# Kernel optimization log

Measured on AMD Instinct MI355X. Metric: run time of the kernel, lower is better.

Reference implementation:

```python
import jax, jax.numpy as jnp
import numpy as np


def setup_inputs() -> dict:
    key = jax.random.key(0)
    k1, k2 = jax.random.split(key)
    B, S, D = 32, 1024, 1024
    text = jax.random.normal(k1, (B, S, D), dtype=jnp.float32)
    W = jax.random.normal(k2, (D, D), dtype=jnp.float32) * (1.0 / np.sqrt(D))
    b = jnp.zeros((D,), dtype=jnp.float32)
    return {"text": text, "W": W, "b": b}


def reference(text, W, b):
    # Q = K = V = Linear(text); torch Linear is x @ W.T + b
    D = W.shape[0]
    qkv = text @ W.T + b  # [B, S, D]
    scale = jnp.asarray(1.0 / np.sqrt(D), dtype=qkv.dtype)
    scores = jnp.einsum("bqd,bkd->bqk", qkv, qkv) * scale  # [B, S, S]
    # F.softmax(H) on a 3D tensor uses torch's legacy implicit dim=0 (batch dim)
    attn = jax.nn.softmax(scores, axis=0)
    out = jnp.einsum("bqk,bkd->bqd", attn, qkv)  # [B, S, D]
    return out
```

## Files before the change

### kernel.cpp

```cpp
#include <hip/hip_runtime.h>
#include <hip/hip_bf16.h>

typedef __attribute__((ext_vector_type(4))) float f32x4;
typedef __attribute__((ext_vector_type(8))) short short8;

static constexpr int BB = 32;
static constexpr int SEQ = 1024;
static constexpr int DIM = 1024;

__device__ __forceinline__ ushort f2bf(float f) {
  union { float f; uint u; } x; x.f = f;
  uint r = x.u + 0x7fffu + ((x.u >> 16) & 1u);
  return (ushort)(r >> 16);
}
__device__ __forceinline__ float bf2f(ushort h) {
  union { uint u; float f; } x; x.u = ((uint)h) << 16; return x.f;
}

__device__ __forceinline__ void async16(const void* g, void* l) {
  __builtin_amdgcn_global_load_lds(
      (const __attribute__((address_space(1))) unsigned int*)g,
      (__attribute__((address_space(3))) unsigned int*)l, 16, 0, 0);
}

#define SCHED0 __builtin_amdgcn_sched_barrier(0)
#define BAR    __builtin_amdgcn_s_barrier()
#define VM(n)  asm volatile("s_waitcnt vmcnt(" #n ")" ::: "memory")

__global__ void cvt_kernel(const float* __restrict__ in, ushort* __restrict__ out, long n4) {
  long i = (long)blockIdx.x * blockDim.x + threadIdx.x;
  const long stride = (long)gridDim.x * blockDim.x;
  for (; i < n4; i += stride) {
    float4 v = reinterpret_cast<const float4*>(in)[i];
    ushort4 o = make_ushort4(f2bf(v.x), f2bf(v.y), f2bf(v.z), f2bf(v.w));
    reinterpret_cast<ushort4*>(out)[i] = o;
  }
}

template<int OUT_BF16, int HAS_BIAS, int TMODE>
__global__ __launch_bounds__(512, 2)
void gemm256(const ushort* __restrict__ A, const ushort* __restrict__ Bt,
             void* __restrict__ Cv, const float* __restrict__ bias,
             ushort* __restrict__ Tout,
             int M, int N, int K, float scale,
             long sA, long sB, long sC)
{
  __shared__ __align__(16) ushort As[2][16384];
  __shared__ __align__(16) ushort Bs[2][16384];

  const int t = threadIdx.x;
  const int z = blockIdx.z;
  const ushort* Ab = A + (long)z * sA;
  const ushort* Bb = Bt + (long)z * sB;
  const int tm = blockIdx.y * 256;
  const int tn = blockIdx.x * 256;

  const int l    = t & 63;
  const int w    = t >> 6;
  const int wrow = w >> 2;
  const int wcol = w & 3;
  const int fr   = l & 15;
  const int g    = l >> 4;
  const int aflip = (fr & 7) << 4;

  const int q0 = (g << 4) ^ aflip;
  const int q1 = (64 + (g << 4)) ^ aflip;
  const char* pA0 = (const char*)As + (wrow << 13) + (fr << 7) + q0;
  const char* pA1 = (const char*)As + (wrow << 13) + (fr << 7) + q1;
  const char* pB0 = (const char*)Bs + (wcol << 12) + (fr << 7) + q0;
  const char* pB1 = (const char*)Bs + (wcol << 12) + (fr << 7) + q1;

  auto ldA = [&](int buf, int mi, int ks) -> short8 {
    const int off = (buf << 15) + ((mi >> 1 & 1) << 14) + ((mi >> 2) << 12) + ((mi & 1) << 11);
    return *(const short8*)((ks ? pA1 : pA0) + off);
  };
  auto ldB = [&](int buf, int ni, int ks) -> short8 {
    const int off = (buf << 15) + ((ni >> 1 & 1) << 14) + ((ni & 1) << 11);
    return *(const short8*)((ks ? pB1 : pB0) + off);
  };

  const long tmK = (long)tm * K;
  const long tnK = (long)tn * K;
  auto soff = [&](int j) {
    const int P  = (j << 13) + (t << 4);
    const int L  = P ^ (((P >> 7) & 7) << 4);
    const int lr = L >> 7;
    const int kb = (L & 127) >> 1;
    return (((lr >> 5) & 3) * 64 + ((lr >> 7) << 5) + (lr & 31)) * K + kb;
  };
  const long ao0 = tmK + soff(0), ao1 = tmK + soff(1), ao2 = tmK + soff(2), ao3 = tmK + soff(3);
  const long bo0 = tnK + soff(0), bo1 = tnK + soff(1), bo2 = tnK + soff(2), bo3 = tnK + soff(3);
  const int t16 = t << 4;
  auto stgA = [&](int buf, int j, long go, int koff) {
    async16(Ab + go + koff, (char*)As + (buf << 15) + (j << 13) + t16);
  };
  auto stgB = [&](int buf, int j, long go, int koff) {
    async16(Bb + go + koff, (char*)Bs + (buf << 15) + (j << 13) + t16);
  };

  f32x4 acc[8][4];
#pragma unroll
  for (int i = 0; i < 8; ++i)
#pragma unroll
    for (int j = 0; j < 4; ++j) acc[i][j] = {0.f, 0.f, 0.f, 0.f};

  short8 a0[4][2], a1[4][2], b0[2][2], b1[2][2];
  constexpr int MI0[4] = {0, 1, 4, 5};
  constexpr int MI1[4] = {2, 3, 6, 7};

#define MFMA_Q(ASET, MIARR, BSET, NIOFF)                                        \
  __builtin_amdgcn_s_setprio(1);                                                \
  _Pragma("unroll") for (int ks = 0; ks < 2; ++ks)                              \
  _Pragma("unroll") for (int s = 0; s < 4; ++s)                                 \
  _Pragma("unroll") for (int ni = 0; ni < 2; ++ni)                              \
    acc[MIARR[s]][ni + NIOFF] = __builtin_amdgcn_mfma_f32_16x16x32_bf16(        \
        ASET[s][ks], BSET[ni][ks], acc[MIARR[s]][ni + NIOFF], 0, 0, 0);         \
  __builtin_amdgcn_s_setprio(0);

  const int NKT = K >> 6;

  stgA(0, 0, ao0, 0);  stgA(0, 1, ao1, 0);
  stgB(0, 0, bo0, 0);  stgB(0, 1, bo1, 0);
  stgB(0, 2, bo2, 0);  stgB(0, 3, bo3, 0);
  stgA(0, 2, ao2, 0);  stgA(0, 3, ao3, 0);
  stgA(1, 0, ao0, 64); stgA(1, 1, ao1, 64);
  stgB(1, 0, bo0, 64); stgB(1, 1, bo1, 64);
  stgB(1, 2, bo2, 64); stgB(1, 3, bo3, 64);
  VM(8);
  BAR;

#pragma unroll
  for (int s = 0; s < 4; ++s) { a0[s][0] = ldA(0, MI0[s], 0); a0[s][1] = ldA(0, MI0[s], 1); }
#pragma unroll
  for (int ni = 0; ni < 2; ++ni) { b0[ni][0] = ldB(0, ni, 0); b0[ni][1] = ldB(0, ni, 1); }

#pragma unroll 2
  for (int kt = 0; kt < NKT; ++kt) {
    const int buf = kt & 1;
    const bool h1 = (kt + 1) < NKT;
    const bool h2 = (kt + 2) < NKT;
    const int k1 = (kt + 1) << 6;
    const int k2 = (kt + 2) << 6;

#pragma unroll
    for (int ni = 0; ni < 2; ++ni) { b1[ni][0] = ldB(buf, ni + 2, 0); b1[ni][1] = ldB(buf, ni + 2, 1); }
    if (h1) { stgA(buf ^ 1, 2, ao2, k1); stgA(buf ^ 1, 3, ao3, k1); }
    SCHED0;
    MFMA_Q(a0, MI0, b0, 0);
    if (kt < NKT - 1) { VM(8); } else { VM(0); }
    BAR;

#pragma unroll
    for (int s = 0; s < 4; ++s) { a1[s][0] = ldA(buf, MI1[s], 0); a1[s][1] = ldA(buf, MI1[s], 1); }
    if (h2) { stgA(buf, 0, ao0, k2); stgA(buf, 1, ao1, k2); }
    SCHED0;
    MFMA_Q(a0, MI0, b1, 2);
    if (kt < NKT - 2) { VM(8); } else if (kt == NKT - 2) { VM(6); }
    BAR;

    if (h1) {
#pragma unroll
      for (int s = 0; s < 4; ++s) { a0[s][0] = ldA(buf ^ 1, MI0[s], 0); a0[s][1] = ldA(buf ^ 1, MI0[s], 1); }
    }
    if (h2) { stgB(buf, 0, bo0, k2); stgB(buf, 1, bo1, k2); }
    SCHED0;
    MFMA_Q(a1, MI1, b0, 0);
    if (kt < NKT - 2) { VM(8); } else if (kt == NKT - 2) { VM(4); }
    BAR;

    if (h1) {
#pragma unroll
      for (int ni = 0; ni < 2; ++ni) { b0[ni][0] = ldB(buf ^ 1, ni, 0); b0[ni][1] = ldB(buf ^ 1, ni, 1); }
    }
    if (h2) { stgB(buf, 2, bo2, k2); stgB(buf, 3, bo3, k2); }
    SCHED0;
    MFMA_Q(a1, MI1, b1, 2);
    if (kt < NKT - 2) { VM(8); } else if (kt == NKT - 2) { VM(2); }
    BAR;
  }
#undef MFMA_Q

  const int cr = g * 4;
#pragma unroll
  for (int mi = 0; mi < 8; ++mi) {
#pragma unroll
    for (int ni = 0; ni < 4; ++ni) {
      const int row = tm + wrow * 128 + mi * 16 + cr;
      const int col = tn + wcol * 64 + ni * 16 + fr;
      const float bv = HAS_BIAS ? bias[col] : 0.0f;
      float v[4];
#pragma unroll
      for (int r = 0; r < 4; ++r) v[r] = acc[mi][ni][r] * scale + bv;
#pragma unroll
      for (int r = 0; r < 4; ++r) {
        const long off = (long)z * sC + (long)(row + r) * N + col;
        if (OUT_BF16) ((ushort*)Cv)[off] = f2bf(v[r]);
        else          ((float*)Cv)[off]  = v[r];
      }
      if (TMODE) {
        ushort4 o = make_ushort4(f2bf(v[0]), f2bf(v[1]), f2bf(v[2]), f2bf(v[3]));
        const long ti = ((long)(row >> 10) << 20) + ((long)col << 10) + (row & 1023);
        *(ushort4*)&Tout[ti] = o;
      }
    }
  }
}

__global__ void softmax_b(ushort* __restrict__ sc) {
  const long SSl = (long)SEQ * SEQ;
  const long e = ((long)blockIdx.x * blockDim.x + threadIdx.x) * 4;
  if (e >= SSl) return;
  uint2 raw[BB];
#pragma unroll
  for (int b = 0; b < BB; ++b) raw[b] = *(const uint2*)&sc[b * SSl + e];
  float mx[4] = {-3.0e38f, -3.0e38f, -3.0e38f, -3.0e38f};
#pragma unroll
  for (int b = 0; b < BB; ++b) {
    const uint lo = raw[b].x, hi = raw[b].y;
    mx[0] = fmaxf(mx[0], bf2f((ushort)(lo & 0xffffu)));
    mx[1] = fmaxf(mx[1], bf2f((ushort)(lo >> 16)));
    mx[2] = fmaxf(mx[2], bf2f((ushort)(hi & 0xffffu)));
    mx[3] = fmaxf(mx[3], bf2f((ushort)(hi >> 16)));
  }
  float sum[4] = {0.f, 0.f, 0.f, 0.f};
#pragma unroll
  for (int b = 0; b < BB; ++b) {
    const uint lo = raw[b].x, hi = raw[b].y;
    const float x0 = __expf(bf2f((ushort)(lo & 0xffffu)) - mx[0]);
    const float x1 = __expf(bf2f((ushort)(lo >> 16))     - mx[1]);
    const float x2 = __expf(bf2f((ushort)(hi & 0xffffu)) - mx[2]);
    const float x3 = __expf(bf2f((ushort)(hi >> 16))     - mx[3]);
    sum[0] += x0; sum[1] += x1; sum[2] += x2; sum[3] += x3;
    raw[b].x = (uint)f2bf(x0) | ((uint)f2bf(x1) << 16);
    raw[b].y = (uint)f2bf(x2) | ((uint)f2bf(x3) << 16);
  }
  const float r0 = 1.0f / sum[0], r1 = 1.0f / sum[1];
  const float r2 = 1.0f / sum[2], r3 = 1.0f / sum[3];
#pragma unroll
  for (int b = 0; b < BB; ++b) {
    const uint lo = raw[b].x, hi = raw[b].y;
    const uint o0 = f2bf(bf2f((ushort)(lo & 0xffffu)) * r0);
    const uint o1 = f2bf(bf2f((ushort)(lo >> 16))     * r1);
    const uint o2 = f2bf(bf2f((ushort)(hi & 0xffffu)) * r2);
    const uint o3 = f2bf(bf2f((ushort)(hi >> 16))     * r3);
    uint2 o; o.x = o0 | (o1 << 16); o.y = o2 | (o3 << 16);
    *(uint2*)&sc[b * SSl + e] = o;
  }
}

extern "C" void kernel_launch(void* const* d_in, const int* in_sizes, int n_in,
                              void* d_out, int out_size, void* d_ws, size_t ws_size,
                              hipStream_t stream) {
  const float* text = (const float*)d_in[0];
  const float* W    = (const float*)d_in[1];
  const float* bias = (const float*)d_in[2];
  float* out = (float*)d_out;

  const long nTxt = (long)BB * SEQ * DIM;
  const long nW   = (long)DIM * DIM;
  const long SSl  = (long)SEQ * SEQ;

  char* ws = (char*)d_ws;
  ushort* qkv   = (ushort*)ws;
  ushort* qkvT  = (ushort*)(ws + nTxt * 2);
  ushort* sc    = (ushort*)(ws + nTxt * 4);
  ushort* textb = sc;
  ushort* Wb    = (ushort*)(ws + nTxt * 6);
  if (ws_size < (size_t)(nTxt * 6 + nW * 2)) return;

  cvt_kernel<<<2048, 256, 0, stream>>>(text, textb, nTxt / 4);
  cvt_kernel<<<256, 256, 0, stream>>>(W, Wb, nW / 4);
  gemm256<1, 1, 1><<<dim3(4, 128, 1), 512, 0, stream>>>(
      textb, Wb, qkv, bias, qkvT, BB * SEQ, DIM, DIM, 1.0f, 0, 0, 0);
  gemm256<1, 0, 0><<<dim3(4, 4, BB), 512, 0, stream>>>(
      qkv, qkv, sc, nullptr, nullptr, SEQ, SEQ, DIM, 0.03125f, SSl, SSl, SSl);
  softmax_b<<<1024, 256, 0, stream>>>(sc);
  gemm256<0, 0, 0><<<dim3(4, 4, BB), 512, 0, stream>>>(
      sc, qkvT, out, nullptr, nullptr, SEQ, DIM, SEQ, 1.0f, SSl, SSl, SSl);
}
```

Before: 376.3 us.

## Exploit score symmetry with triangular-tile GEMM and XCD-aware block remapping

Adds a 128x128-tile GEMM that computes only the lower-triangular tiles of the symmetric Q·Q^T score matrix and mirrors each off-diagonal tile via transposed bf16 stores, roughly halving the score GEMM's MFMA work. All GEMMs now use a 1D grid with a block-index swizzle that spreads consecutive logical tiles across the 8 XCDs for better L2 locality. The transposed mirror writes are strided and uncoalesced, and the triangular index decode uses a per-block loop.

```diff
diff --git a/kernel.cpp b/kernel.cpp
--- a/kernel.cpp
+++ b/kernel.cpp
@@ -42,19 +42,25 @@
 void gemm256(const ushort* __restrict__ A, const ushort* __restrict__ Bt,
              void* __restrict__ Cv, const float* __restrict__ bias,
              ushort* __restrict__ Tout,
-             int M, int N, int K, float scale,
+             int nx, int ny, int K, float scale,
              long sA, long sB, long sC)
 {
   __shared__ __align__(16) ushort As[2][16384];
   __shared__ __align__(16) ushort Bs[2][16384];
 
-  const int t = threadIdx.x;
-  const int z = blockIdx.z;
+  const int lg = (blockIdx.x & 7) * (gridDim.x >> 3) + (blockIdx.x >> 3);
+  const int tx = lg % nx;
+  const int rr = lg / nx;
+  const int ty = rr % ny;
+  const int z  = rr / ny;
+  const int N  = nx * 256;
+  const int tm = ty * 256;
+  const int tn = tx * 256;
+
   const ushort* Ab = A + (long)z * sA;
   const ushort* Bb = Bt + (long)z * sB;
-  const int tm = blockIdx.y * 256;
-  const int tn = blockIdx.x * 256;
-
+
+  const int t = threadIdx.x;
   const int l    = t & 63;
   const int w    = t >> 6;
   const int wrow = w >> 2;
@@ -206,6 +212,109 @@
   }
 }
 
+template<int OUT_BF16, int HAS_BIAS, int SYM>
+__global__ void gemm_bt(const ushort* __restrict__ A, const ushort* __restrict__ Bt,
+                        void* __restrict__ Cv, const float* __restrict__ bias,
+                        int nx, int ny, int K, float scale,
+                        long sA, long sB, long sC)
+{
+  __shared__ ushort As[2][128 * 32];
+  __shared__ ushort Bs[2][128 * 32];
+
+  const int lg = (blockIdx.x & 7) * (gridDim.x >> 3) + (blockIdx.x >> 3);
+  int tx, ty, z;
+  if (SYM) {
+    const int P = nx * (nx + 1) / 2;
+    z = lg / P;
+    const int u = lg - z * P;
+    int i = 0;
+    while ((i + 1) * (i + 2) / 2 <= u) ++i;
+    ty = i; tx = u - i * (i + 1) / 2;
+  } else {
+    tx = lg % nx;
+    const int r = lg / nx;
+    ty = r % ny;
+    z = r / ny;
+  }
+  const int N = nx * 128;
+  const int tm = ty * 128;
+  const int tn = tx * 128;
+
+  const ushort* Ab = A + (long)z * sA;
+  const ushort* Bb = Bt + (long)z * sB;
+
+  const int t = threadIdx.x;
+  const int l  = t & 63;
+  const int w  = t >> 6;
+  const int wm = (w >> 1) * 64;
+  const int wn = (w & 1) * 64;
+  const int fr = l & 15;
+  const int g  = l >> 4;
+  const int kp = (((g + (fr >> 1)) & 3) << 3);
+
+  f32x4 acc[4][4];
+#pragma unroll
+  for (int i = 0; i < 4; ++i)
+#pragma unroll
+    for (int j = 0; j < 4; ++j) acc[i][j] = {0.f, 0.f, 0.f, 0.f};
+
+  auto stage = [&](int buf, int k0) {
+#pragma unroll
+    for (int it = 0; it < 2; ++it) {
+      const int idx = t + it * 256;
+      const int r   = idx >> 2;
+      const int sl  = ((idx & 3) - (r >> 1)) & 3;
+      const int kb  = sl * 8;
+      async16(Ab + (long)(tm + r) * K + (k0 + kb), &As[buf][idx * 8]);
+      async16(Bb + (long)(tn + r) * K + (k0 + kb), &Bs[buf][idx * 8]);
+    }
+  };
+
+  const int nk = K >> 5;
+  stage(0, 0);
+  __syncthreads();
+  for (int kt = 0; kt < nk; ++kt) {
+    const int buf = kt & 1;
+    if (kt + 1 < nk) stage(buf ^ 1, (kt + 1) << 5);
+    short8 af[4], bfr[4];
+#pragma unroll
+    for (int f = 0; f < 4; ++f) {
+      af[f]  = *(const short8*)&As[buf][(wm + f * 16 + fr) * 32 + kp];
+      bfr[f] = *(const short8*)&Bs[buf][(wn + f * 16 + fr) * 32 + kp];
+    }
+#pragma unroll
+    for (int i = 0; i < 4; ++i)
+#pragma unroll
+      for (int j = 0; j < 4; ++j)
+        acc[i][j] = __builtin_amdgcn_mfma_f32_16x16x32_bf16(af[i], bfr[j], acc[i][j], 0, 0, 0);
+    __syncthreads();
+  }
+
+  const int cr = g * 4;
+#pragma unroll
+  for (int i = 0; i < 4; ++i) {
+#pragma unroll
+    for (int j = 0; j < 4; ++j) {
+      const int row = tm + wm + i * 16 + cr;
+      const int col = tn + wn + j * 16 + fr;
+      const float bv = HAS_BIAS ? bias[col] : 0.0f;
+      float v[4];
+#pragma unroll
+      for (int r = 0; r < 4; ++r) v[r] = acc[i][j][r] * scale + bv;
+#pragma unroll
+      for (int r = 0; r < 4; ++r) {
+        const long off = (long)z * sC + (long)(row + r) * N + col;
+        if (OUT_BF16) ((ushort*)Cv)[off] = f2bf(v[r]);
+        else          ((float*)Cv)[off]  = v[r];
+      }
+      if (SYM && tx != ty) {
+        ushort4 o = make_ushort4(f2bf(v[0]), f2bf(v[1]), f2bf(v[2]), f2bf(v[3]));
+        *(ushort4*)((ushort*)Cv + (long)z * sC + (long)col * N + row) = o;
+      }
+    }
+  }
+}
+
 __global__ void softmax_b(ushort* __restrict__ sc) {
   const long SSl = (long)SEQ * SEQ;
   const long e = ((long)blockIdx.x * blockDim.x + threadIdx.x) * 4;
@@ -270,11 +379,11 @@
 
   cvt_kernel<<<2048, 256, 0, stream>>>(text, textb, nTxt / 4);
   cvt_kernel<<<256, 256, 0, stream>>>(W, Wb, nW / 4);
-  gemm256<1, 1, 1><<<dim3(4, 128, 1), 512, 0, stream>>>(
-      textb, Wb, qkv, bias, qkvT, BB * SEQ, DIM, DIM, 1.0f, 0, 0, 0);
-  gemm256<1, 0, 0><<<dim3(4, 4, BB), 512, 0, stream>>>(
-      qkv, qkv, sc, nullptr, nullptr, SEQ, SEQ, DIM, 0.03125f, SSl, SSl, SSl);
+  gemm256<1, 1, 1><<<512, 512, 0, stream>>>(
+      textb, Wb, qkv, bias, qkvT, 4, 128, DIM, 1.0f, 0, 0, 0);
+  gemm_bt<1, 0, 1><<<1152, 256, 0, stream>>>(
+      qkv, qkv, sc, nullptr, 8, 8, DIM, 0.03125f, SSl, SSl, SSl);
   softmax_b<<<1024, 256, 0, stream>>>(sc);
-  gemm256<0, 0, 0><<<dim3(4, 4, BB), 512, 0, stream>>>(
-      sc, qkvT, out, nullptr, nullptr, SEQ, DIM, SEQ, 1.0f, SSl, SSl, SSl);
-}
+  gemm256<0, 0, 0><<<512, 512, 0, stream>>>(
+      sc, qkvT, out, nullptr, nullptr, 4, 4, SEQ, 1.0f, SSl, SSl, SSl);
+}
```

After: 348.9 us. -7.3%, faster.
